# Kernel tuning notes

Measured on AMD Instinct MI355X. Metric: run time of the kernel, lower is better.

Reference implementation:

```python
import jax, jax.numpy as jnp
import numpy as np

G, B, K, D = 16384, 4, 2, 64
NEG = -1e30


def _mlp3(x, w1, b1, w2, b2, w3, b3):
    # MLP: linear->relu x3 (BatchNorm defined but unused in original forward)
    h = jax.nn.relu(x @ w1 + b1)
    h = jax.nn.relu(h @ w2 + b2)
    return jax.nn.relu(h @ w3 + b3)


def setup_inputs() -> dict:
    key = jax.random.key(0)
    ks = jax.random.split(key, 32)

    def lin(k, fan_in, fan_out):
        k1, k2 = jax.random.split(k)
        s = 1.0 / np.sqrt(fan_in)
        w = jax.random.uniform(k1, (fan_in, fan_out), jnp.float32, -s, s)
        b = jax.random.uniform(k2, (fan_out,), jnp.float32, -s, s)
        return w, b

    inp = {}
    inp['ap_feat'] = jax.random.normal(ks[0], (G, B, 1), jnp.float32)
    inp['e_feat'] = jax.random.normal(ks[1], (G, B, K, 2), jnp.float32)
    inp['w_pre_ap'], inp['b_pre_ap'] = lin(ks[2], 1, D)
    inp['w_pre_edge'], inp['b_pre_edge'] = lin(ks[3], 2, D)
    # mlp_update_5 (AP-side neighbor messages), _6 (UE-side), _7 (edge update)
    inp['w5_1'], inp['b5_1'] = lin(ks[4], 2 * D, D)
    inp['w5_2'], inp['b5_2'] = lin(ks[5], D, D)
    inp['w5_3'], inp['b5_3'] = lin(ks[6], D, D)
    inp['w6_1'], inp['b6_1'] = lin(ks[7], 2 * D, D)
    inp['w6_2'], inp['b6_2'] = lin(ks[8], D, D)
    inp['w6_3'], inp['b6_3'] = lin(ks[9], D, D)
    inp['w7_1'], inp['b7_1'] = lin(ks[10], 2 * D, D)
    inp['w7_2'], inp['b7_2'] = lin(ks[11], D, D)
    inp['w7_3'], inp['b7_3'] = lin(ks[12], D, D)
    inp['w_post'], inp['b_post'] = lin(ks[13], D, 2)
    return inp


def _edge_conv(e, a, w5_1, b5_1, w5_2, b5_2, w5_3, b5_3,
               w6_1, b6_1, w6_2, b6_2, w6_3, b6_3,
               w7_1, b7_1, w7_2, b7_2, w7_3, b7_3):
    # e: [G,B,K,D] AP2UE edge hid; a: [G,B,D] AP hid.
    # M1[g,b,j] = mlp5(cat(a[g,b], e[g,b,j])) -- same-AP neighbor edges
    x1 = jnp.concatenate([jnp.broadcast_to(a[:, :, None, :], e.shape), e], axis=-1)  # [G,B,K,2D]
    M1 = _mlp3(x1, w5_1, b5_1, w5_2, b5_2, w5_3, b5_3)  # [G,B,K,D]
    # M2[g,b,bp,k] = mlp6(cat(a[g,b], e[g,bp,k])) -- same-UE neighbor edges
    # (original uses the SRC AP feature here too). Split first linear to
    # avoid materializing the [G,B,B,K,2D] concat.
    h = jax.nn.relu(
        (a @ w6_1[:D])[:, :, None, None, :]
        + (e @ w6_1[D:])[:, None, :, :, :]
        + b6_1)  # [G,B,B,K,D]
    h = jax.nn.relu(h @ w6_2 + b6_2)
    M2 = jax.nn.relu(h @ w6_3 + b6_3)  # [G,B,Bp,K,D]
    # masked max excluding the edge itself
    eyeK = jnp.eye(K, dtype=bool)  # [k, j]
    m1max = jnp.max(jnp.where(eyeK[None, None, :, :, None], NEG,
                              M1[:, :, None, :, :]), axis=3)  # [G,B,K,D]
    eyeB = jnp.eye(B, dtype=bool)  # [b, bp]
    m2max = jnp.max(jnp.where(eyeB[None, :, :, None, None], NEG, M2), axis=2)  # [G,B,K,D]
    agg = jnp.maximum(m1max, m2max)
    # new edge feature: mlp7(cat(agg, e_hid))
    return _mlp3(jnp.concatenate([agg, e], axis=-1),
                 w7_1, b7_1, w7_2, b7_2, w7_3, b7_3)


def reference(ap_feat, e_feat, w_pre_ap, b_pre_ap, w_pre_edge, b_pre_edge,
              w5_1, b5_1, w5_2, b5_2, w5_3, b5_3,
              w6_1, b6_1, w6_2, b6_2, w6_3, b6_3,
              w7_1, b7_1, w7_2, b7_2, w7_3, b7_3,
              w_post, b_post):
    # PreLayer (live branches only: AP nodes and AP2UE edges; APConv/UEConv
    # write node 'new' which is never read, so UE/UE2AP branches are dead).
    a = jax.nn.relu(ap_feat @ w_pre_ap + b_pre_ap)   # [G,B,D]
    e = jax.nn.relu(e_feat @ w_pre_edge + b_pre_edge)  # [G,B,K,D]
    # two UpdateLayers (shared weights: ModuleList([UpdateLayer()]*2) + global MLPs)
    for _ in range(2):
        e = _edge_conv(e, a, w5_1, b5_1, w5_2, b5_2, w5_3, b5_3,
                       w6_1, b6_1, w6_2, b6_2, w6_3, b6_3,
                       w7_1, b7_1, w7_2, b7_2, w7_3, b7_3)
    out = e @ w_post + b_post  # [G,B,K,2]
    r, im = out[..., 0], out[..., 1]
    # norm_func: per-graph [B,K] complex matrix, each row (over K) L2-normalized
    n = jnp.sqrt(jnp.sum(r * r + im * im, axis=-1, keepdims=True))
    return jnp.stack([r / n, im / n], axis=-1)  # [G,B,K,2]
```

## Files before the change

kernel.cpp:

```cpp
#include <hip/hip_runtime.h>


typedef unsigned short u16;
typedef unsigned int   u32;
typedef __attribute__((ext_vector_type(8))) short short8_t;
typedef __attribute__((ext_vector_type(2))) short short2v;
typedef __attribute__((ext_vector_type(4))) float floatx4;

#define OFF_W51 0
#define OFF_W61 8192
#define OFF_W71 16384
#define OFF_W52 24576
#define OFF_W53 28672
#define OFF_W62 32768
#define OFF_W63 36864
#define OFF_W72 40960
#define OFF_W73 45056
#define WS_U16  49152

#define CB51 0
#define CB52 64
#define CB53 128
#define CB61 192
#define CB62 256
#define CB63 320
#define CB71 384
#define CB72 448
#define CB73 512
#define CWPO 576
#define CBPO 704
#define CWPA 768
#define CBPA 832
#define CWPE 896
#define CBPE 1024
#define CSZ  1088

#define PW_U16 1536

struct Params {
  const float *ap, *ef;
  const float *wpa, *bpa, *wpe, *bpe;
  const float *w51, *b51, *w52, *b52, *w53, *b53;
  const float *w61, *b61, *w62, *b62, *w63, *b63;
  const float *w71, *b71, *w72, *b72, *w73, *b73;
  const float *wpost, *bpost;
  float *out;
  int gtot;
};

__device__ __forceinline__ u32 pk2(float a, float b) {
  const u32 ua = __float_as_uint(a) + 0x8000u;
  const u32 ub = __float_as_uint(b) + 0x8000u;
  return __builtin_amdgcn_perm(ub, ua, 0x07060302u);
}
__device__ __forceinline__ float blo(u32 v) { return __uint_as_float(v << 16); }
__device__ __forceinline__ float bhi(u32 v) { return __uint_as_float(v & 0xffff0000u); }
__device__ __forceinline__ u32 pkmax(u32 a, u32 b) {
  const short2v r = __builtin_elementwise_max(__builtin_bit_cast(short2v, a),
                                              __builtin_bit_cast(short2v, b));
  return __builtin_bit_cast(u32, r);
}
__device__ __forceinline__ u32 ror16(u32 x) { return (x >> 16) | (x << 16); }
__device__ __forceinline__ float sel4(int i, float x0, float x1, float x2, float x3) {
  const float lo = (i & 1) ? x1 : x0;
  const float hi = (i & 1) ? x3 : x2;
  return (i & 2) ? hi : lo;
}

__device__ __forceinline__ floatx4 mfma16(short8_t a, short8_t b, floatx4 c) {
  return __builtin_amdgcn_mfma_f32_16x16x32_bf16(a, b, c, 0, 0, 0);
}
__device__ __forceinline__ short8_t ldA(const u16* buf, int l) {
  return *(const short8_t*)(buf + l * 8);
}

template<int TSTRIDE>
__device__ __forceinline__ void layerK64R(floatx4* acc, short8_t a0, short8_t a1,
                                          const u16* B, int l) {
#pragma unroll
  for (int t = 0; t < 4; ++t) {
    const short8_t b0 = *(const short8_t*)(B + (t * TSTRIDE + 0) * 512 + l * 8);
    const short8_t b1 = *(const short8_t*)(B + (t * TSTRIDE + 1) * 512 + l * 8);
    acc[t] = mfma16(a0, b0, acc[t]);
    acc[t] = mfma16(a1, b1, acc[t]);
  }
}

__device__ __forceinline__ void layerK128R(floatx4* acc, short8_t a0, short8_t a1,
                                           short8_t a2, short8_t a3,
                                           const u16* B, int l) {
  short8_t a[4] = {a0, a1, a2, a3};
#pragma unroll
  for (int t = 0; t < 4; ++t)
#pragma unroll
    for (int h = 0; h < 4; ++h)
      acc[t] = mfma16(a[h], *(const short8_t*)(B + (t * 4 + h) * 512 + l * 8), acc[t]);
}

__device__ __forceinline__ void scatter_relu_bf16(u16* dst, const floatx4* acc, int q, int n) {
#pragma unroll
  for (int t = 0; t < 4; ++t) {
    const int kk = (t & 1) * 2 + (n >> 3);
    u16* base = dst + (t >> 1) * 512 + (n & 7);
    const u32 v01 = pk2(fmaxf(acc[t][0], 0.f), fmaxf(acc[t][1], 0.f));
    const u32 v23 = pk2(fmaxf(acc[t][2], 0.f), fmaxf(acc[t][3], 0.f));
    base[(4 * q + 0 + 16 * kk) * 8] = (u16)v01;
    base[(4 * q + 1 + 16 * kk) * 8] = (u16)(v01 >> 16);
    base[(4 * q + 2 + 16 * kk) * 8] = (u16)v23;
    base[(4 * q + 3 + 16 * kk) * 8] = (u16)(v23 >> 16);
  }
}

__device__ __forceinline__ void scatter_bf16(u16* dst, const floatx4* acc, int q, int n) {
#pragma unroll
  for (int t = 0; t < 4; ++t) {
    const int kk = (t & 1) * 2 + (n >> 3);
    u16* base = dst + (t >> 1) * 512 + (n & 7);
    const u32 v01 = pk2(acc[t][0], acc[t][1]);
    const u32 v23 = pk2(acc[t][2], acc[t][3]);
    base[(4 * q + 0 + 16 * kk) * 8] = (u16)v01;
    base[(4 * q + 1 + 16 * kk) * 8] = (u16)(v01 >> 16);
    base[(4 * q + 2 + 16 * kk) * 8] = (u16)v23;
    base[(4 * q + 3 + 16 * kk) * 8] = (u16)(v23 >> 16);
  }
}

__device__ __forceinline__ void scatter_pk(u16* dst, const u32* src, int q, int n) {
#pragma unroll
  for (int t = 0; t < 4; ++t) {
    const int kk = (t & 1) * 2 + (n >> 3);
    u16* base = dst + (t >> 1) * 512 + (n & 7);
#pragma unroll
    for (int half = 0; half < 2; ++half) {
      const u32 v = src[2 * t + half];
      base[(4 * q + 2 * half + 0 + 16 * kk) * 8] = (u16)v;
      base[(4 * q + 2 * half + 1 + 16 * kk) * 8] = (u16)(v >> 16);
    }
  }
}

__device__ __forceinline__ void scatter_aP(u16* dst, const floatx4* acc, int q, int n,
                                           const float* cb61) {
#pragma unroll
  for (int t = 0; t < 4; ++t) {
    const int kk = (t & 1) * 2 + (n >> 3);
    u16* base = dst + (t >> 1) * 256 + (n & 7);
    const float bv = cb61[16 * t + n];
    const u32 v = pk2(acc[t][0] + bv, acc[t][2] + bv);
    base[(2 * q + 0 + 8 * kk) * 8] = (u16)v;
    base[(2 * q + 1 + 8 * kk) * 8] = (u16)(v >> 16);
  }
}

__device__ __forceinline__ void init_accL(floatx4* acc, const float* cb, int n) {
#pragma unroll
  for (int t = 0; t < 4; ++t) {
    const float b = cb[16 * t + n];
    floatx4 v; v[0] = b; v[1] = b; v[2] = b; v[3] = b;
    acc[t] = v;
  }
}

struct frag2 { short8_t f0, f1; };

__device__ __forceinline__ frag2 make_a(float apv, int q, const float* sc) {
  frag2 r;
#pragma unroll
  for (int h = 0; h < 2; ++h) {
    const int fb = 32 * h + 8 * q;
    const float4 wa0 = *(const float4*)(sc + CWPA + fb);
    const float4 wa1 = *(const float4*)(sc + CWPA + fb + 4);
    const float4 ba0 = *(const float4*)(sc + CBPA + fb);
    const float4 ba1 = *(const float4*)(sc + CBPA + fb + 4);
    uint4 pa;
    pa.x = pk2(fmaxf(fmaf(apv, wa0.x, ba0.x), 0.f), fmaxf(fmaf(apv, wa0.y, ba0.y), 0.f));
    pa.y = pk2(fmaxf(fmaf(apv, wa0.z, ba0.z), 0.f), fmaxf(fmaf(apv, wa0.w, ba0.w), 0.f));
    pa.z = pk2(fmaxf(fmaf(apv, wa1.x, ba1.x), 0.f), fmaxf(fmaf(apv, wa1.y, ba1.y), 0.f));
    pa.w = pk2(fmaxf(fmaf(apv, wa1.z, ba1.z), 0.f), fmaxf(fmaf(apv, wa1.w, ba1.w), 0.f));
    if (h == 0) r.f0 = __builtin_bit_cast(short8_t, pa);
    else        r.f1 = __builtin_bit_cast(short8_t, pa);
  }
  return r;
}

#define NBLK 256
#define NWAVE 16
#define PPW  2

__global__ __attribute__((amdgpu_waves_per_eu(4, 4), amdgpu_num_vgpr(128)))
__launch_bounds__(1024, 4)
void hetgnn_mfma(Params p) {
  __shared__ __align__(16) u16   sW[WS_U16];
  __shared__ __align__(16) u16   sAct[NWAVE * PW_U16];
  __shared__ __align__(16) float sConst[CSZ];

  const int tid  = threadIdx.x;
  const int wave = tid >> 6;
  const int l    = tid & 63;
  const int q    = l >> 4;
  const int n    = l & 15;

  {
    const float* mats[9] = {p.w51, p.w61, p.w71, p.w52, p.w53, p.w62, p.w63, p.w72, p.w73};
    for (int fi = wave; fi < 96; fi += NWAVE) {
      const float* W;
      int t, h;
      if (fi < 48) { W = mats[fi >> 4]; const int loc = fi & 15; t = loc >> 2; h = loc & 3; }
      else { const int j = fi - 48; W = mats[3 + (j >> 3)]; const int loc = j & 7; t = loc >> 1; h = loc & 1; }
      const int nn = 16 * t + n;
      const int k0 = 32 * h + q * 8;
      float w[8];
#pragma unroll
      for (int j = 0; j < 8; ++j) w[j] = W[(k0 + j) * 64 + nn];
      uint4 o;
      o.x = pk2(w[0], w[1]); o.y = pk2(w[2], w[3]);
      o.z = pk2(w[4], w[5]); o.w = pk2(w[6], w[7]);
      *(uint4*)(sW + fi * 512 + l * 8) = o;
    }
  }
  if (tid < 64) {
    sConst[CB51 + tid] = p.b51[tid];
    sConst[CB52 + tid] = p.b52[tid];
    sConst[CB53 + tid] = p.b53[tid];
    sConst[CB61 + tid] = p.b61[tid];
    sConst[CB62 + tid] = p.b62[tid];
    sConst[CB63 + tid] = p.b63[tid];
    sConst[CB71 + tid] = p.b71[tid];
    sConst[CB72 + tid] = p.b72[tid];
    sConst[CB73 + tid] = p.b73[tid];
    sConst[CWPA + tid] = p.wpa[tid];
    sConst[CBPA + tid] = p.bpa[tid];
    sConst[CBPE + tid] = p.bpe[tid];
  }
  if (tid < 128) {
    sConst[CWPO + tid] = p.wpost[tid];
    sConst[CWPE + tid] = p.wpe[tid];
  }
  if (tid < 2) sConst[CBPO + tid] = p.bpost[tid];
  __syncthreads();

  u16* BUF = sAct + wave * PW_U16;
  u16* aPb = BUF + 1024;

  const int wslot = blockIdx.x * NWAVE + wave;

  for (int pi = 0; pi < PPW; ++pi) {
    const int g0 = (wslot * PPW + pi) * 2;
    if (g0 + 2 > p.gtot) break;

    const float apv = p.ap[(g0 + (n >> 3)) * 4 + ((n >> 1) & 3)];
    const frag2 A = make_a(apv, q, sConst);
    short8_t e0, e1;
    {
      const float f0 = p.ef[(g0 + (n >> 3)) * 16 + (n & 7) * 2];
      const float f1 = p.ef[(g0 + (n >> 3)) * 16 + (n & 7) * 2 + 1];
#pragma unroll
      for (int h = 0; h < 2; ++h) {
        const int fb = 32 * h + 8 * q;
        const float4 w00 = *(const float4*)(sConst + CWPE + fb);
        const float4 w01 = *(const float4*)(sConst + CWPE + fb + 4);
        const float4 w10 = *(const float4*)(sConst + CWPE + 64 + fb);
        const float4 w11 = *(const float4*)(sConst + CWPE + 64 + fb + 4);
        const float4 be0 = *(const float4*)(sConst + CBPE + fb);
        const float4 be1 = *(const float4*)(sConst + CBPE + fb + 4);
        uint4 pe;
        pe.x = pk2(fmaxf(fmaf(f0, w00.x, fmaf(f1, w10.x, be0.x)), 0.f),
                   fmaxf(fmaf(f0, w00.y, fmaf(f1, w10.y, be0.y)), 0.f));
        pe.y = pk2(fmaxf(fmaf(f0, w00.z, fmaf(f1, w10.z, be0.z)), 0.f),
                   fmaxf(fmaf(f0, w00.w, fmaf(f1, w10.w, be0.w)), 0.f));
        pe.z = pk2(fmaxf(fmaf(f0, w01.x, fmaf(f1, w11.x, be1.x)), 0.f),
                   fmaxf(fmaf(f0, w01.y, fmaf(f1, w11.y, be1.y)), 0.f));
        pe.w = pk2(fmaxf(fmaf(f0, w01.z, fmaf(f1, w11.z, be1.z)), 0.f),
                   fmaxf(fmaf(f0, w01.w, fmaf(f1, w11.w, be1.w)), 0.f));
        if (h == 0) e0 = __builtin_bit_cast(short8_t, pe);
        else        e1 = __builtin_bit_cast(short8_t, pe);
      }
    }

    {
      floatx4 accA[4];
#pragma unroll
      for (int t = 0; t < 4; ++t) { accA[t][0] = 0.f; accA[t][1] = 0.f; accA[t][2] = 0.f; accA[t][3] = 0.f; }
      layerK64R<4>(accA, A.f0, A.f1, sW + OFF_W61, l);
      scatter_aP(aPb, accA, q, n, sConst + CB61);
    }

#pragma unroll 1
    for (int it = 0; it < 2; ++it) {
      if (it == 1) { e0 = ldA(BUF, l); e1 = ldA(BUF + 512, l); }

      u32 m1p[8];
      {
        floatx4 acc[4]; init_accL(acc, sConst + CB51, n);
        layerK128R(acc, A.f0, A.f1, e0, e1, sW + OFF_W51, l);
        scatter_relu_bf16(BUF, acc, q, n);
        floatx4 acc2[4]; init_accL(acc2, sConst + CB52, n);
        layerK64R<2>(acc2, ldA(BUF, l), ldA(BUF + 512, l), sW + OFF_W52, l);
        scatter_relu_bf16(BUF, acc2, q, n);
        floatx4 acc3[4]; init_accL(acc3, sConst + CB53, n);
        layerK64R<2>(acc3, ldA(BUF, l), ldA(BUF + 512, l), sW + OFF_W53, l);
#pragma unroll
        for (int t = 0; t < 4; ++t) {
          m1p[2 * t + 0] = pk2(acc3[t][0], acc3[t][1]);
          m1p[2 * t + 1] = pk2(acc3[t][2], acc3[t][3]);
        }
      }

      u32 m2p[8];
      {
        floatx4 accE[4];
#pragma unroll
        for (int t = 0; t < 4; ++t) { accE[t][0] = 0.f; accE[t][1] = 0.f; accE[t][2] = 0.f; accE[t][3] = 0.f; }
        layerK64R<4>(accE, e0, e1, sW + OFF_W61 + 2 * 512, l);
        scatter_bf16(BUF, accE, q, n);

        const int d = n >> 1;
        const int b_ln = d & 3;
        short8_t hf0[3], hf1[3];
#pragma unroll
        for (int j = 0; j < 3; ++j) {
          const int bp = (j >= b_ln) ? (j + 1) : j;
          const int re = (n & 8) + bp * 2 + (n & 1);
#pragma unroll
          for (int h = 0; h < 2; ++h) {
            const uint4 av = *(const uint4*)(aPb + h * 256 + (d + 8 * q) * 8);
            const uint4 ev = *(const uint4*)(BUF + h * 512 + (re + 16 * q) * 8);
            uint4 ph;
            ph.x = pk2(fmaxf(blo(av.x) + blo(ev.x), 0.f),
                       fmaxf(bhi(av.x) + bhi(ev.x), 0.f));
            ph.y = pk2(fmaxf(blo(av.y) + blo(ev.y), 0.f),
                       fmaxf(bhi(av.y) + bhi(ev.y), 0.f));
            ph.z = pk2(fmaxf(blo(av.z) + blo(ev.z), 0.f),
                       fmaxf(bhi(av.z) + bhi(ev.z), 0.f));
            ph.w = pk2(fmaxf(blo(av.w) + blo(ev.w), 0.f),
                       fmaxf(bhi(av.w) + bhi(ev.w), 0.f));
            if (h == 0) hf0[j] = __builtin_bit_cast(short8_t, ph);
            else        hf1[j] = __builtin_bit_cast(short8_t, ph);
          }
        }
#pragma unroll
        for (int j = 0; j < 3; ++j) {
          floatx4 acc2[4]; init_accL(acc2, sConst + CB62, n);
          layerK64R<2>(acc2, hf0[j], hf1[j], sW + OFF_W62, l);
          scatter_relu_bf16(BUF, acc2, q, n);
          floatx4 acc3[4]; init_accL(acc3, sConst + CB63, n);
          layerK64R<2>(acc3, ldA(BUF, l), ldA(BUF + 512, l), sW + OFF_W63, l);
#pragma unroll
          for (int t = 0; t < 4; ++t) {
#pragma unroll
            for (int h = 0; h < 2; ++h) {
              const u32 cand = pk2(acc3[t][2 * h], acc3[t][2 * h + 1]);
              m2p[2 * t + h] = (j == 0) ? cand : pkmax(m2p[2 * t + h], cand);
            }
          }
        }
      }

      {
        u32 agp[8];
#pragma unroll
        for (int i = 0; i < 8; ++i)
          agp[i] = pkmax(pkmax(ror16(m1p[i]), m2p[i]), 0u);
        scatter_pk(BUF, agp, q, n);
        floatx4 acc[4]; init_accL(acc, sConst + CB71, n);
        layerK128R(acc, ldA(BUF, l), ldA(BUF + 512, l), e0, e1, sW + OFF_W71, l);
        scatter_relu_bf16(BUF, acc, q, n);
        floatx4 acc2[4]; init_accL(acc2, sConst + CB72, n);
        layerK64R<2>(acc2, ldA(BUF, l), ldA(BUF + 512, l), sW + OFF_W72, l);
        scatter_relu_bf16(BUF, acc2, q, n);
        floatx4 acc3[4]; init_accL(acc3, sConst + CB73, n);
        layerK64R<2>(acc3, ldA(BUF, l), ldA(BUF + 512, l), sW + OFF_W73, l);

        if (it == 0) {
          scatter_relu_bf16(BUF, acc3, q, n);
        } else {
          float prr[4] = {0.f, 0.f, 0.f, 0.f}, pii[4] = {0.f, 0.f, 0.f, 0.f};
#pragma unroll
          for (int t = 0; t < 4; ++t) {
            const float wr = sConst[CWPO + (16 * t + n) * 2];
            const float wi = sConst[CWPO + (16 * t + n) * 2 + 1];
#pragma unroll
            for (int r = 0; r < 4; ++r) {
              const float e = fmaxf(acc3[t][r], 0.f);
              prr[r] = fmaf(e, wr, prr[r]);
              pii[r] = fmaf(e, wi, pii[r]);
            }
          }
          const float bpR = sConst[CBPO], bpI = sConst[CBPO + 1];
#pragma unroll
          for (int r = 0; r < 4; ++r) {
#pragma unroll
            for (int off = 1; off < 16; off <<= 1) {
              prr[r] += __shfl_xor(prr[r], off, 16);
              pii[r] += __shfl_xor(pii[r], off, 16);
            }
            prr[r] += bpR;
            pii[r] += bpI;
          }
          const int r = n >> 1, c = n & 1, rp = r ^ 1;
          const float pr_r  = sel4(r,  prr[0], prr[1], prr[2], prr[3]);
          const float pi_r  = sel4(r,  pii[0], pii[1], pii[2], pii[3]);
          const float pr_rp = sel4(rp, prr[0], prr[1], prr[2], prr[3]);
          const float pi_rp = sel4(rp, pii[0], pii[1], pii[2], pii[3]);
          const float num = c ? pi_r : pr_r;
          const float n2  = pr_r * pr_r + pi_r * pi_r + pr_rp * pr_rp + pi_rp * pi_rp;
          if (n < 8) p.out[g0 * 16 + (4 * q + r) * 2 + c] = num / sqrtf(n2);
        }
      }
    }
  }
}

extern "C" void kernel_launch(void* const* d_in, const int* in_sizes, int n_in,
                              void* d_out, int out_size, void* d_ws, size_t ws_size,
                              hipStream_t stream) {
  Params p;
  p.ap    = (const float*)d_in[0];
  p.ef    = (const float*)d_in[1];
  p.wpa   = (const float*)d_in[2];  p.bpa   = (const float*)d_in[3];
  p.wpe   = (const float*)d_in[4];  p.bpe   = (const float*)d_in[5];
  p.w51   = (const float*)d_in[6];  p.b51   = (const float*)d_in[7];
  p.w52   = (const float*)d_in[8];  p.b52   = (const float*)d_in[9];
  p.w53   = (const float*)d_in[10]; p.b53   = (const float*)d_in[11];
  p.w61   = (const float*)d_in[12]; p.b61   = (const float*)d_in[13];
  p.w62   = (const float*)d_in[14]; p.b62   = (const float*)d_in[15];
  p.w63   = (const float*)d_in[16]; p.b63   = (const float*)d_in[17];
  p.w71   = (const float*)d_in[18]; p.b71   = (const float*)d_in[19];
  p.w72   = (const float*)d_in[20]; p.b72   = (const float*)d_in[21];
  p.w73   = (const float*)d_in[22]; p.b73   = (const float*)d_in[23];
  p.wpost = (const float*)d_in[24]; p.bpost = (const float*)d_in[25];
  p.out   = (float*)d_out;
  p.gtot  = in_sizes[0] / 4;

  hipLaunchKernelGGL(hetgnn_mfma, dim3(NBLK), dim3(1024), 0, stream, p);
}
```

Baseline: 159.8 us.

## Interleave two independent graph-pair streams per wave to raise MFMA ILP

Each wave now processes two graph pairs (X and Y) at once, interleaving their MFMA chains so every B-fragment load from LDS is shared by two matrix multiplies. This hides MFMA latency and halves weight reads per graph. To pay for the doubled register and LDS working set, the block shrinks from 16 to 8 waves and occupancy drops from 4 to 2 waves per EU. The total work per launch stays the same (256 blocks × 8 waves × 4 pairs). The trade-off is lower occupancy and higher register pressure, which may cause spills.

Result: slower. 163.9 us (+2.6%).

```diff
diff --git a/kernel.cpp b/kernel.cpp
--- a/kernel.cpp
+++ b/kernel.cpp
@@ -35,7 +35,7 @@
 #define CBPE 1024
 #define CSZ  1088
 
-#define PW_U16 1536
+#define PW_U16 3072
 
 struct Params {
   const float *ap, *ef;
@@ -75,26 +75,32 @@
 }
 
 template<int TSTRIDE>
-__device__ __forceinline__ void layerK64R(floatx4* acc, short8_t a0, short8_t a1,
-                                          const u16* B, int l) {
+__device__ __forceinline__ void layerK64R2(floatx4* aX, floatx4* aY,
+                                           short8_t x0, short8_t x1,
+                                           short8_t y0, short8_t y1,
+                                           const u16* B, int l) {
 #pragma unroll
   for (int t = 0; t < 4; ++t) {
     const short8_t b0 = *(const short8_t*)(B + (t * TSTRIDE + 0) * 512 + l * 8);
     const short8_t b1 = *(const short8_t*)(B + (t * TSTRIDE + 1) * 512 + l * 8);
-    acc[t] = mfma16(a0, b0, acc[t]);
-    acc[t] = mfma16(a1, b1, acc[t]);
-  }
-}
-
-__device__ __forceinline__ void layerK128R(floatx4* acc, short8_t a0, short8_t a1,
-                                           short8_t a2, short8_t a3,
-                                           const u16* B, int l) {
-  short8_t a[4] = {a0, a1, a2, a3};
+    aX[t] = mfma16(x0, b0, aX[t]);
+    aY[t] = mfma16(y0, b0, aY[t]);
+    aX[t] = mfma16(x1, b1, aX[t]);
+    aY[t] = mfma16(y1, b1, aY[t]);
+  }
+}
+
+__device__ __forceinline__ void layerK128R2(floatx4* aX, floatx4* aY,
+                                            const short8_t* fx, const short8_t* fy,
+                                            const u16* B, int l) {
 #pragma unroll
   for (int t = 0; t < 4; ++t)
 #pragma unroll
-    for (int h = 0; h < 4; ++h)
-      acc[t] = mfma16(a[h], *(const short8_t*)(B + (t * 4 + h) * 512 + l * 8), acc[t]);
+    for (int h = 0; h < 4; ++h) {
+      const short8_t b = *(const short8_t*)(B + (t * 4 + h) * 512 + l * 8);
+      aX[t] = mfma16(fx[h], b, aX[t]);
+      aY[t] = mfma16(fy[h], b, aY[t]);
+    }
 }
 
 __device__ __forceinline__ void scatter_relu_bf16(u16* dst, const floatx4* acc, int q, int n) {
@@ -159,6 +165,10 @@
     floatx4 v; v[0] = b; v[1] = b; v[2] = b; v[3] = b;
     acc[t] = v;
   }
+}
+__device__ __forceinline__ void init_acc0(floatx4* acc) {
+#pragma unroll
+  for (int t = 0; t < 4; ++t) { acc[t][0] = 0.f; acc[t][1] = 0.f; acc[t][2] = 0.f; acc[t][3] = 0.f; }
 }
 
 struct frag2 { short8_t f0, f1; };
@@ -183,12 +193,107 @@
   return r;
 }
 
+__device__ __forceinline__ void prelayer(frag2& A, short8_t& e0, short8_t& e1,
+                                         const Params& p, const float* sc,
+                                         int g0, int q, int n) {
+  const float apv = p.ap[(g0 + (n >> 3)) * 4 + ((n >> 1) & 3)];
+  A = make_a(apv, q, sc);
+  const float f0 = p.ef[(g0 + (n >> 3)) * 16 + (n & 7) * 2];
+  const float f1 = p.ef[(g0 + (n >> 3)) * 16 + (n & 7) * 2 + 1];
+#pragma unroll
+  for (int h = 0; h < 2; ++h) {
+    const int fb = 32 * h + 8 * q;
+    const float4 w00 = *(const float4*)(sc + CWPE + fb);
+    const float4 w01 = *(const float4*)(sc + CWPE + fb + 4);
+    const float4 w10 = *(const float4*)(sc + CWPE + 64 + fb);
+    const float4 w11 = *(const float4*)(sc + CWPE + 64 + fb + 4);
+    const float4 be0 = *(const float4*)(sc + CBPE + fb);
+    const float4 be1 = *(const float4*)(sc + CBPE + fb + 4);
+    uint4 pe;
+    pe.x = pk2(fmaxf(fmaf(f0, w00.x, fmaf(f1, w10.x, be0.x)), 0.f),
+               fmaxf(fmaf(f0, w00.y, fmaf(f1, w10.y, be0.y)), 0.f));
+    pe.y = pk2(fmaxf(fmaf(f0, w00.z, fmaf(f1, w10.z, be0.z)), 0.f),
+               fmaxf(fmaf(f0, w00.w, fmaf(f1, w10.w, be0.w)), 0.f));
+    pe.z = pk2(fmaxf(fmaf(f0, w01.x, fmaf(f1, w11.x, be1.x)), 0.f),
+               fmaxf(fmaf(f0, w01.y, fmaf(f1, w11.y, be1.y)), 0.f));
+    pe.w = pk2(fmaxf(fmaf(f0, w01.z, fmaf(f1, w11.z, be1.z)), 0.f),
+               fmaxf(fmaf(f0, w01.w, fmaf(f1, w11.w, be1.w)), 0.f));
+    if (h == 0) e0 = __builtin_bit_cast(short8_t, pe);
+    else        e1 = __builtin_bit_cast(short8_t, pe);
+  }
+}
+
+__device__ __forceinline__ void build_h(short8_t* hf0, short8_t* hf1,
+                                        const u16* aPb, const u16* BUF,
+                                        int q, int n) {
+  const int d = n >> 1;
+  const int b_ln = d & 3;
+  const uint4 av0 = *(const uint4*)(aPb + 0 * 256 + (d + 8 * q) * 8);
+  const uint4 av1 = *(const uint4*)(aPb + 1 * 256 + (d + 8 * q) * 8);
+#pragma unroll
+  for (int j = 0; j < 3; ++j) {
+    const int bp = (j >= b_ln) ? (j + 1) : j;
+    const int re = (n & 8) + bp * 2 + (n & 1);
+#pragma unroll
+    for (int h = 0; h < 2; ++h) {
+      const uint4 av = h ? av1 : av0;
+      const uint4 ev = *(const uint4*)(BUF + h * 512 + (re + 16 * q) * 8);
+      uint4 ph;
+      ph.x = pk2(fmaxf(blo(av.x) + blo(ev.x), 0.f),
+                 fmaxf(bhi(av.x) + bhi(ev.x), 0.f));
+      ph.y = pk2(fmaxf(blo(av.y) + blo(ev.y), 0.f),
+                 fmaxf(bhi(av.y) + bhi(ev.y), 0.f));
+      ph.z = pk2(fmaxf(blo(av.z) + blo(ev.z), 0.f),
+                 fmaxf(bhi(av.z) + bhi(ev.z), 0.f));
+      ph.w = pk2(fmaxf(blo(av.w) + blo(ev.w), 0.f),
+                 fmaxf(bhi(av.w) + bhi(ev.w), 0.f));
+      if (h == 0) hf0[j] = __builtin_bit_cast(short8_t, ph);
+      else        hf1[j] = __builtin_bit_cast(short8_t, ph);
+    }
+  }
+}
+
+__device__ __forceinline__ void epilogue(const floatx4* acc3, const float* sc,
+                                         float* out, int g0, int q, int n, bool ok) {
+  float prr[4] = {0.f, 0.f, 0.f, 0.f}, pii[4] = {0.f, 0.f, 0.f, 0.f};
+#pragma unroll
+  for (int t = 0; t < 4; ++t) {
+    const float wr = sc[CWPO + (16 * t + n) * 2];
+    const float wi = sc[CWPO + (16 * t + n) * 2 + 1];
+#pragma unroll
+    for (int r = 0; r < 4; ++r) {
+      const float e = fmaxf(acc3[t][r], 0.f);
+      prr[r] = fmaf(e, wr, prr[r]);
+      pii[r] = fmaf(e, wi, pii[r]);
+    }
+  }
+  const float bpR = sc[CBPO], bpI = sc[CBPO + 1];
+#pragma unroll
+  for (int r = 0; r < 4; ++r) {
+#pragma unroll
+    for (int off = 1; off < 16; off <<= 1) {
+      prr[r] += __shfl_xor(prr[r], off, 16);
+      pii[r] += __shfl_xor(pii[r], off, 16);
+    }
+    prr[r] += bpR;
+    pii[r] += bpI;
+  }
+  const int r = n >> 1, c = n & 1, rp = r ^ 1;
+  const float pr_r  = sel4(r,  prr[0], prr[1], prr[2], prr[3]);
+  const float pi_r  = sel4(r,  pii[0], pii[1], pii[2], pii[3]);
+  const float pr_rp = sel4(rp, prr[0], prr[1], prr[2], prr[3]);
+  const float pi_rp = sel4(rp, pii[0], pii[1], pii[2], pii[3]);
+  const float num = c ? pi_r : pr_r;
+  const float n2  = pr_r * pr_r + pi_r * pi_r + pr_rp * pr_rp + pi_rp * pi_rp;
+  if (ok && n < 8) out[g0 * 16 + (4 * q + r) * 2 + c] = num / sqrtf(n2);
+}
+
 #define NBLK 256
-#define NWAVE 16
+#define NWAVE 8
 #define PPW  2
 
-__global__ __attribute__((amdgpu_waves_per_eu(4, 4), amdgpu_num_vgpr(128)))
-__launch_bounds__(1024, 4)
+__global__ __launch_bounds__(512, 2)
+__attribute__((amdgpu_waves_per_eu(2, 2)))
 void hetgnn_mfma(Params p) {
   __shared__ __align__(16) u16   sW[WS_U16];
   __shared__ __align__(16) u16   sAct[NWAVE * PW_U16];
@@ -201,12 +306,14 @@
   const int n    = l & 15;
 
   {
-    const float* mats[9] = {p.w51, p.w61, p.w71, p.w52, p.w53, p.w62, p.w63, p.w72, p.w73};
     for (int fi = wave; fi < 96; fi += NWAVE) {
-      const float* W;
-      int t, h;
-      if (fi < 48) { W = mats[fi >> 4]; const int loc = fi & 15; t = loc >> 2; h = loc & 3; }
-      else { const int j = fi - 48; W = mats[3 + (j >> 3)]; const int loc = j & 7; t = loc >> 1; h = loc & 1; }
+      int t, h, mi;
+      if (fi < 48) { mi = fi >> 4; const int loc = fi & 15; t = loc >> 2; h = loc & 3; }
+      else { const int j = fi - 48; mi = 3 + (j >> 3); const int loc = j & 7; t = loc >> 1; h = loc & 1; }
+      const float* W =
+          (mi == 0) ? p.w51 : (mi == 1) ? p.w61 : (mi == 2) ? p.w71 :
+          (mi == 3) ? p.w52 : (mi == 4) ? p.w53 : (mi == 5) ? p.w62 :
+          (mi == 6) ? p.w63 : (mi == 7) ? p.w72 : p.w73;
       const int nn = 16 * t + n;
       const int k0 = 32 * h + q * 8;
       float w[8];
@@ -239,172 +346,157 @@
   if (tid < 2) sConst[CBPO + tid] = p.bpost[tid];
   __syncthreads();
 
-  u16* BUF = sAct + wave * PW_U16;
-  u16* aPb = BUF + 1024;
+  u16* BUF0 = sAct + wave * PW_U16;
+  u16* aPb0 = BUF0 + 1024;
+  u16* BUF1 = BUF0 + 1536;
+  u16* aPb1 = BUF1 + 1024;
 
   const int wslot = blockIdx.x * NWAVE + wave;
 
+#pragma unroll 1
   for (int pi = 0; pi < PPW; ++pi) {
-    const int g0 = (wslot * PPW + pi) * 2;
-    if (g0 + 2 > p.gtot) break;
-
-    const float apv = p.ap[(g0 + (n >> 3)) * 4 + ((n >> 1) & 3)];
-    const frag2 A = make_a(apv, q, sConst);
-    short8_t e0, e1;
+    const int g0X = (wslot * 4 + 2 * pi) * 2;
+    const int g0Y = g0X + 2;
+    if (g0X + 2 > p.gtot) break;
+    const bool okY = (g0Y + 2 <= p.gtot);
+    const int gY  = okY ? g0Y : g0X;
+
+    frag2 AX, AY;
+    short8_t ex0, ex1, ey0, ey1;
+    prelayer(AX, ex0, ex1, p, sConst, g0X, q, n);
+    prelayer(AY, ey0, ey1, p, sConst, gY,  q, n);
+
     {
-      const float f0 = p.ef[(g0 + (n >> 3)) * 16 + (n & 7) * 2];
-      const float f1 = p.ef[(g0 + (n >> 3)) * 16 + (n & 7) * 2 + 1];
-#pragma unroll
-      for (int h = 0; h < 2; ++h) {
-        const int fb = 32 * h + 8 * q;
-        const float4 w00 = *(const float4*)(sConst + CWPE + fb);
-        const float4 w01 = *(const float4*)(sConst + CWPE + fb + 4);
-        const float4 w10 = *(const float4*)(sConst + CWPE + 64 + fb);
-        const float4 w11 = *(const float4*)(sConst + CWPE + 64 + fb + 4);
-        const float4 be0 = *(const float4*)(sConst + CBPE + fb);
-        const float4 be1 = *(const float4*)(sConst + CBPE + fb + 4);
-        uint4 pe;
-        pe.x = pk2(fmaxf(fmaf(f0, w00.x, fmaf(f1, w10.x, be0.x)), 0.f),
-                   fmaxf(fmaf(f0, w00.y, fmaf(f1, w10.y, be0.y)), 0.f));
-        pe.y = pk2(fmaxf(fmaf(f0, w00.z, fmaf(f1, w10.z, be0.z)), 0.f),
-                   fmaxf(fmaf(f0, w00.w, fmaf(f1, w10.w, be0.w)), 0.f));
-        pe.z = pk2(fmaxf(fmaf(f0, w01.x, fmaf(f1, w11.x, be1.x)), 0.f),
-                   fmaxf(fmaf(f0, w01.y, fmaf(f1, w11.y, be1.y)), 0.f));
-        pe.w = pk2(fmaxf(fmaf(f0, w01.z, fmaf(f1, w11.z, be1.z)), 0.f),
-                   fmaxf(fmaf(f0, w01.w, fmaf(f1, w11.w, be1.w)), 0.f));
-        if (h == 0) e0 = __builtin_bit_cast(short8_t, pe);
-        else        e1 = __builtin_bit_cast(short8_t, pe);
-      }
-    }
-
-    {
-      floatx4 accA[4];
-#pragma unroll
-      for (int t = 0; t < 4; ++t) { accA[t][0] = 0.f; accA[t][1] = 0.f; accA[t][2] = 0.f; accA[t][3] = 0.f; }
-      layerK64R<4>(accA, A.f0, A.f1, sW + OFF_W61, l);
-      scatter_aP(aPb, accA, q, n, sConst + CB61);
+      floatx4 aaX[4], aaY[4];
+      init_acc0(aaX); init_acc0(aaY);
+      layerK64R2<4>(aaX, aaY, AX.f0, AX.f1, AY.f0, AY.f1, sW + OFF_W61, l);
+      scatter_aP(aPb0, aaX, q, n, sConst + CB61);
+      scatter_aP(aPb1, aaY, q, n, sConst + CB61);
     }
 
 #pragma unroll 1
     for (int it = 0; it < 2; ++it) {
-      if (it == 1) { e0 = ldA(BUF, l); e1 = ldA(BUF + 512, l); }
-
-      u32 m1p[8];
+      if (it == 1) {
+        ex0 = ldA(BUF0, l); ex1 = ldA(BUF0 + 512, l);
+        ey0 = ldA(BUF1, l); ey1 = ldA(BUF1 + 512, l);
+      }
+
+      u32 m1pX[8], m1pY[8];
       {
-        floatx4 acc[4]; init_accL(acc, sConst + CB51, n);
-        layerK128R(acc, A.f0, A.f1, e0, e1, sW + OFF_W51, l);
-        scatter_relu_bf16(BUF, acc, q, n);
-        floatx4 acc2[4]; init_accL(acc2, sConst + CB52, n);
-        layerK64R<2>(acc2, ldA(BUF, l), ldA(BUF + 512, l), sW + OFF_W52, l);
-        scatter_relu_bf16(BUF, acc2, q, n);
-        floatx4 acc3[4]; init_accL(acc3, sConst + CB53, n);
-        layerK64R<2>(acc3, ldA(BUF, l), ldA(BUF + 512, l), sW + OFF_W53, l);
+        floatx4 aX[4], aY[4];
+        init_accL(aX, sConst + CB51, n); init_accL(aY, sConst + CB51, n);
+        const short8_t fx[4] = {AX.f0, AX.f1, ex0, ex1};
+        const short8_t fy[4] = {AY.f0, AY.f1, ey0, ey1};
+        layerK128R2(aX, aY, fx, fy, sW + OFF_W51, l);
+        scatter_relu_bf16(BUF0, aX, q, n);
+        scatter_relu_bf16(BUF1, aY, q, n);
+        floatx4 bX[4], bY[4];
+        init_accL(bX, sConst + CB52, n); init_accL(bY, sConst + CB52, n);
+        {
+          const short8_t gx0 = ldA(BUF0, l), gx1 = ldA(BUF0 + 512, l);
+          const short8_t gy0 = ldA(BUF1, l), gy1 = ldA(BUF1 + 512, l);
+          layerK64R2<2>(bX, bY, gx0, gx1, gy0, gy1, sW + OFF_W52, l);
+        }
+        scatter_relu_bf16(BUF0, bX, q, n);
+        scatter_relu_bf16(BUF1, bY, q, n);
+        floatx4 cX[4], cY[4];
+        init_accL(cX, sConst + CB53, n); init_accL(cY, sConst + CB53, n);
+        {
+          const short8_t gx0 = ldA(BUF0, l), gx1 = ldA(BUF0 + 512, l);
+          const short8_t gy0 = ldA(BUF1, l), gy1 = ldA(BUF1 + 512, l);
+          layerK64R2<2>(cX, cY, gx0, gx1, gy0, gy1, sW + OFF_W53, l);
+        }
 #pragma unroll
         for (int t = 0; t < 4; ++t) {
-          m1p[2 * t + 0] = pk2(acc3[t][0], acc3[t][1]);
-          m1p[2 * t + 1] = pk2(acc3[t][2], acc3[t][3]);
+          m1pX[2 * t + 0] = pk2(cX[t][0], cX[t][1]);
+          m1pX[2 * t + 1] = pk2(cX[t][2], cX[t][3]);
+          m1pY[2 * t + 0] = pk2(cY[t][0], cY[t][1]);
+          m1pY[2 * t + 1] = pk2(cY[t][2], cY[t][3]);
         }
       }
 
-      u32 m2p[8];
+      u32 m2pX[8], m2pY[8];
       {
-        floatx4 accE[4];
-#pragma unroll
-        for (int t = 0; t < 4; ++t) { accE[t][0] = 0.f; accE[t][1] = 0.f; accE[t][2] = 0.f; accE[t][3] = 0.f; }
-        layerK64R<4>(accE, e0, e1, sW + OFF_W61 + 2 * 512, l);
-        scatter_bf16(BUF, accE, q, n);
-
-        const int d = n >> 1;
-        const int b_ln = d & 3;
-        short8_t hf0[3], hf1[3];
+        floatx4 eX[4], eY[4];
+        init_acc0(eX); init_acc0(eY);
+        layerK64R2<4>(eX, eY, ex0, ex1, ey0, ey1, sW + OFF_W61 + 2 * 512, l);
+        scatter_bf16(BUF0, eX, q, n);
+        scatter_bf16(BUF1, eY, q, n);
+
+        short8_t hfX0[3], hfX1[3], hfY0[3], hfY1[3];
+        build_h(hfX0, hfX1, aPb0, BUF0, q, n);
+        build_h(hfY0, hfY1, aPb1, BUF1, q, n);
+
 #pragma unroll
         for (int j = 0; j < 3; ++j) {
-          const int bp = (j >= b_ln) ? (j + 1) : j;
-          const int re = (n & 8) + bp * 2 + (n & 1);
-#pragma unroll
-          for (int h = 0; h < 2; ++h) {
-            const uint4 av = *(const uint4*)(aPb + h * 256 + (d + 8 * q) * 8);
-            const uint4 ev = *(const uint4*)(BUF + h * 512 + (re + 16 * q) * 8);
-            uint4 ph;
-            ph.x = pk2(fmaxf(blo(av.x) + blo(ev.x), 0.f),
-                       fmaxf(bhi(av.x) + bhi(ev.x), 0.f));
-            ph.y = pk2(fmaxf(blo(av.y) + blo(ev.y), 0.f),
-                       fmaxf(bhi(av.y) + bhi(ev.y), 0.f));
-            ph.z = pk2(fmaxf(blo(av.z) + blo(ev.z), 0.f),
-                       fmaxf(bhi(av.z) + bhi(ev.z), 0.f));
-            ph.w = pk2(fmaxf(blo(av.w) + blo(ev.w), 0.f),
-                       fmaxf(bhi(av.w) + bhi(ev.w), 0.f));
-            if (h == 0) hf0[j] = __builtin_bit_cast(short8_t, ph);
-            else        hf1[j] = __builtin_bit_cast(short8_t, ph);
+          floatx4 uX[4], uY[4];
+          init_accL(uX, sConst + CB62, n); init_accL(uY, sConst + CB62, n);
+          layerK64R2<2>(uX, uY, hfX0[j], hfX1[j], hfY0[j], hfY1[j], sW + OFF_W62, l);
+          scatter_relu_bf16(BUF0, uX, q, n);
+          scatter_relu_bf16(BUF1, uY, q, n);
+          floatx4 vX[4], vY[4];
+          init_accL(vX, sConst + CB63, n); init_accL(vY, sConst + CB63, n);
+          {
+            const short8_t gx0 = ldA(BUF0, l), gx1 = ldA(BUF0 + 512, l);
+            const short8_t gy0 = ldA(BUF1, l), gy1 = ldA(BUF1 + 512, l);
+            layerK64R2<2>(vX, vY, gx0, gx1, gy0, gy1, sW + OFF_W63, l);
           }
-        }
-#pragma unroll
-        for (int j = 0; j < 3; ++j) {
-          floatx4 acc2[4]; init_accL(acc2, sConst + CB62, n);
-          layerK64R<2>(acc2, hf0[j], hf1[j], sW + OFF_W62, l);
-          scatter_relu_bf16(BUF, acc2, q, n);
-          floatx4 acc3[4]; init_accL(acc3, sConst + CB63, n);
-          layerK64R<2>(acc3, ldA(BUF, l), ldA(BUF + 512, l), sW + OFF_W63, l);
 #pragma unroll
           for (int t = 0; t < 4; ++t) {
 #pragma unroll
             for (int h = 0; h < 2; ++h) {
-              const u32 cand = pk2(acc3[t][2 * h], acc3[t][2 * h + 1]);
-              m2p[2 * t + h] = (j == 0) ? cand : pkmax(m2p[2 * t + h], cand);
+              const u32 cX = pk2(vX[t][2 * h], vX[t][2 * h + 1]);
+              const u32 cY = pk2(vY[t][2 * h], vY[t][2 * h + 1]);
+              m2pX[2 * t + h] = (j == 0) ? cX : pkmax(m2pX[2 * t + h], cX);
+              m2pY[2 * t + h] = (j == 0) ? cY : pkmax(m2pY[2 * t + h], cY);
             }
           }
         }
       }
 
       {
-        u32 agp[8];
-#pragma unroll
-        for (int i = 0; i < 8; ++i)
-          agp[i] = pkmax(pkmax(ror16(m1p[i]), m2p[i]), 0u);
-        scatter_pk(BUF, agp, q, n);
-        floatx4 acc[4]; init_accL(acc, sConst + CB71, n);
-        layerK128R(acc, ldA(BUF, l), ldA(BUF + 512, l), e0, e1, sW + OFF_W71, l);
-        scatter_relu_bf16(BUF, acc, q, n);
-        floatx4 acc2[4]; init_accL(acc2, sConst + CB72, n);
-        layerK64R<2>(acc2, ldA(BUF, l), ldA(BUF + 512, l), sW + OFF_W72, l);
-        scatter_relu_bf16(BUF, acc2, q, n);
-        floatx4 acc3[4]; init_accL(acc3, sConst + CB73, n);
-        layerK64R<2>(acc3, ldA(BUF, l), ldA(BUF + 512, l), sW + OFF_W73, l);
+        u32 agX[8], agY[8];
+#pragma unroll
+        for (int i = 0; i < 8; ++i) {
+          agX[i] = pkmax(pkmax(ror16(m1pX[i]), m2pX[i]), 0u);
+          agY[i] = pkmax(pkmax(ror16(m1pY[i]), m2pY[i]), 0u);
+        }
+        scatter_pk(BUF0, agX, q, n);
+        scatter_pk(BUF1, agY, q, n);
+        floatx4 aX[4], aY[4];
+        init_accL(aX, sConst + CB71, n); init_accL(aY, sConst + CB71, n);
+        {
+          const short8_t gx0 = ldA(BUF0, l), gx1 = ldA(BUF0 + 512, l);
+          const short8_t gy0 = ldA(BUF1, l), gy1 = ldA(BUF1 + 512, l);
+          const short8_t fx[4] = {gx0, gx1, ex0, ex1};
+          const short8_t fy[4] = {gy0, gy1, ey0, ey1};
+          layerK128R2(aX, aY, fx, fy, sW + OFF_W71, l);
+        }
+        scatter_relu_bf16(BUF0, aX, q, n);
+        scatter_relu_bf16(BUF1, aY, q, n);
+        floatx4 bX[4], bY[4];
+        init_accL(bX, sConst + CB72, n); init_accL(bY, sConst + CB72, n);
+        {
+          const short8_t gx0 = ldA(BUF0, l), gx1 = ldA(BUF0 + 512, l);
+          const short8_t gy0 = ldA(BUF1, l), gy1 = ldA(BUF1 + 512, l);
+          layerK64R2<2>(bX, bY, gx0, gx1, gy0, gy1, sW + OFF_W72, l);
+        }
+        scatter_relu_bf16(BUF0, bX, q, n);
+        scatter_relu_bf16(BUF1, bY, q, n);
+        floatx4 cX[4], cY[4];
+        init_accL(cX, sConst + CB73, n); init_accL(cY, sConst + CB73, n);
+        {
+          const short8_t gx0 = ldA(BUF0, l), gx1 = ldA(BUF0 + 512, l);
+          const short8_t gy0 = ldA(BUF1, l), gy1 = ldA(BUF1 + 512, l);
+          layerK64R2<2>(cX, cY, gx0, gx1, gy0, gy1, sW + OFF_W73, l);
+        }
 
         if (it == 0) {
-          scatter_relu_bf16(BUF, acc3, q, n);
+          scatter_relu_bf16(BUF0, cX, q, n);
+          scatter_relu_bf16(BUF1, cY, q, n);
         } else {
-          float prr[4] = {0.f, 0.f, 0.f, 0.f}, pii[4] = {0.f, 0.f, 0.f, 0.f};
-#pragma unroll
-          for (int t = 0; t < 4; ++t) {
-            const float wr = sConst[CWPO + (16 * t + n) * 2];
-            const float wi = sConst[CWPO + (16 * t + n) * 2 + 1];
-#pragma unroll
-            for (int r = 0; r < 4; ++r) {
-              const float e = fmaxf(acc3[t][r], 0.f);
-              prr[r] = fmaf(e, wr, prr[r]);
-              pii[r] = fmaf(e, wi, pii[r]);
-            }
-          }
-          const float bpR = sConst[CBPO], bpI = sConst[CBPO + 1];
-#pragma unroll
-          for (int r = 0; r < 4; ++r) {
-#pragma unroll
-            for (int off = 1; off < 16; off <<= 1) {
-              prr[r] += __shfl_xor(prr[r], off, 16);
-              pii[r] += __shfl_xor(pii[r], off, 16);
-            }
-            prr[r] += bpR;
-            pii[r] += bpI;
-          }
-          const int r = n >> 1, c = n & 1, rp = r ^ 1;
-          const float pr_r  = sel4(r,  prr[0], prr[1], prr[2], prr[3]);
-          const float pi_r  = sel4(r,  pii[0], pii[1], pii[2], pii[3]);
-          const float pr_rp = sel4(rp, prr[0], prr[1], prr[2], prr[3]);
-          const float pi_rp = sel4(rp, pii[0], pii[1], pii[2], pii[3]);
-          const float num = c ? pi_r : pr_r;
-          const float n2  = pr_r * pr_r + pi_r * pi_r + pr_rp * pr_rp + pi_rp * pi_rp;
-          if (n < 8) p.out[g0 * 16 + (4 * q + r) * 2 + c] = num / sqrtf(n2);
+          epilogue(cX, sConst, p.out, g0X, q, n, true);
+          epilogue(cY, sConst, p.out, g0Y, q, n, okY);
         }
       }
     }
@@ -432,5 +524,5 @@
   p.out   = (float*)d_out;
   p.gtot  = in_sizes[0] / 4;
 
-  hipLaunchKernelGGL(hetgnn_mfma, dim3(NBLK), dim3(1024), 0, stream, p);
-}
+  hipLaunchKernelGGL(hetgnn_mfma, dim3(NBLK), dim3(512), 0, stream, p);
+}
```
